# Performance work log

Measured on AMD Instinct MI355X. Metric: run time of the kernel, lower is better.

Reference implementation:

```python
import jax, jax.numpy as jnp
import numpy as np

N_NODES = 50000
N_EDGES = 1000000
C = 32          # nchannels (multiplicity of each irrep)
NBESSEL = 8
WEIGHT_NUMEL = 3 * C  # three uvu paths: 0e->0e, 0e->1o, 0e->2e


def setup_inputs() -> dict:
    key = jax.random.key(0)
    ks = jax.random.split(key, 12)
    inp = {
        "lenght": jax.random.uniform(ks[0], (N_EDGES, NBESSEL), dtype=jnp.float32),
        "node_features": jax.random.normal(ks[1], (N_NODES, C), dtype=jnp.float32),
        "edge_attributes": jax.random.normal(ks[2], (N_EDGES, 9), dtype=jnp.float32),
        "edge_index": jax.random.randint(ks[3], (2, N_EDGES), 0, N_NODES, dtype=jnp.int64),
        # FullyConnectedNet([8, 6, 6, 6, 96]) weights (e3nn stores unnormalized W, divides by sqrt(fan_in))
        "fcn_w0": jax.random.normal(ks[4], (NBESSEL, 6), dtype=jnp.float32),
        "fcn_w1": jax.random.normal(ks[5], (6, 6), dtype=jnp.float32),
        "fcn_w2": jax.random.normal(ks[6], (6, 6), dtype=jnp.float32),
        "fcn_w3": jax.random.normal(ks[7], (6, WEIGHT_NUMEL), dtype=jnp.float32),
        # equivariant Linear irreps_mid -> irreps_out: one [C, C] mixing matrix per l in {0,1,2}
        "lin_w0": jax.random.normal(ks[8], (C, C), dtype=jnp.float32),
        "lin_w1": jax.random.normal(ks[9], (C, C), dtype=jnp.float32),
        "lin_w2": jax.random.normal(ks[10], (C, C), dtype=jnp.float32),
    }
    return inp


def _fcn(x, w0, w1, w2, w3):
    # e3nn FullyConnectedNet: normalized linear layers with SiLU on hidden layers
    for w in (w0, w1, w2):
        x = jax.nn.silu((x @ w) * (1.0 / np.float32(np.sqrt(w.shape[0]))))
    return (x @ w3) * (1.0 / np.float32(np.sqrt(w3.shape[0])))


def reference(lenght, node_features, edge_attributes, edge_index,
              fcn_w0, fcn_w1, fcn_w2, fcn_w3, lin_w0, lin_w1, lin_w2):
    sender = edge_index[0]
    receiver = edge_index[1]
    num_nodes = node_features.shape[0]
    c = node_features.shape[1]
    e = lenght.shape[0]

    # per-edge tensor-product weights: [E, 3C]
    tp_w = _fcn(lenght, fcn_w0, fcn_w1, fcn_w2, fcn_w3)
    w0, w1, w2 = tp_w[:, :c], tp_w[:, c:2 * c], tp_w[:, 2 * c:]

    x = node_features[sender]                       # gather: [E, C]
    y0 = edge_attributes[:, 0:1]                    # 0e: [E, 1]
    y1 = edge_attributes[:, 1:4]                    # 1o: [E, 3]
    y2 = edge_attributes[:, 4:9]                    # 2e: [E, 5]

    # uvu tensor product, CG for 0e x l -> l is identity
    m0 = w0 * x * y0                                # [E, C]
    m1 = (w1 * x)[:, :, None] * y1[:, None, :]      # [E, C, 3]
    m2 = (w2 * x)[:, :, None] * y2[:, None, :]      # [E, C, 5]
    mij = jnp.concatenate(
        [m0, m1.reshape(e, 3 * c), m2.reshape(e, 5 * c)], axis=1)  # [E, 9C]

    # scatter_sum over receivers
    msg = jax.ops.segment_sum(mij, receiver, num_segments=num_nodes)  # [N, 9C]

    # equivariant Linear (per-l channel mixing, 1/sqrt(fan_in) normalization)
    inv = 1.0 / np.float32(np.sqrt(c))
    o0 = (msg[:, :c] @ lin_w0) * inv                                   # [N, C]
    o1 = jnp.einsum('nci,cd->ndi', msg[:, c:4 * c].reshape(num_nodes, c, 3), lin_w1) * inv
    o2 = jnp.einsum('nci,cd->ndi', msg[:, 4 * c:].reshape(num_nodes, c, 5), lin_w2) * inv
    return jnp.concatenate(
        [o0, o1.reshape(num_nodes, 3 * c), o2.reshape(num_nodes, 5 * c)], axis=1)
```

## Files before the change

### kernel.cpp

```cpp
#include <hip/hip_runtime.h>
#include <math.h>

#define N_NODES 50000
#define N_EDGES 1000000
#define CCH     32
#define ROW     288
#define SCAN_BLOCKS 196
#define REC_PAD 64

__global__ __launch_bounds__(256) void hist_kernel(
    const int* __restrict__ edge_index, int* __restrict__ deg)
{
    const int e = blockIdx.x * 256 + threadIdx.x;
    if (e >= N_EDGES) return;
    atomicAdd(&deg[edge_index[N_EDGES + e]], 1);
}

__global__ __launch_bounds__(256) void scan_local_kernel(
    const int* __restrict__ deg, int* __restrict__ lexcl, int* __restrict__ blocksum)
{
    __shared__ int s[256];
    const int t = threadIdx.x;
    const int gid = blockIdx.x * 256 + t;
    const int v = (gid < N_NODES) ? deg[gid] : 0;
    s[t] = v;
    __syncthreads();
    for (int ofs = 1; ofs < 256; ofs <<= 1) {
        int w = (t >= ofs) ? s[t - ofs] : 0;
        __syncthreads();
        s[t] += w;
        __syncthreads();
    }
    if (gid < N_NODES) lexcl[gid] = s[t] - v;
    if (t == 255) blocksum[blockIdx.x] = s[255];
}

__global__ __launch_bounds__(256) void scan_top_kernel(
    const int* __restrict__ blocksum, int* __restrict__ blockpref)
{
    __shared__ int s[256];
    const int t = threadIdx.x;
    const int v = (t < SCAN_BLOCKS) ? blocksum[t] : 0;
    s[t] = v;
    __syncthreads();
    for (int ofs = 1; ofs < 256; ofs <<= 1) {
        int w = (t >= ofs) ? s[t - ofs] : 0;
        __syncthreads();
        s[t] += w;
        __syncthreads();
    }
    if (t < SCAN_BLOCKS) blockpref[t] = s[t] - v;
}

__global__ __launch_bounds__(256) void scan_addback_kernel(
    const int* __restrict__ lexcl, const int* __restrict__ blockpref,
    int* __restrict__ offset, int* __restrict__ cursor)
{
    const int gid = blockIdx.x * 256 + threadIdx.x;
    if (gid >= N_NODES) return;
    const int base = blockpref[blockIdx.x] + lexcl[gid];
    offset[gid] = base;
    cursor[gid] = base;
}

__global__ __launch_bounds__(256) void pack_kernel(
    const float* __restrict__ lenght,
    const float* __restrict__ edge_attr,
    const int*   __restrict__ edge_index,
    const float* __restrict__ fw0,
    const float* __restrict__ fw1,
    const float* __restrict__ fw2,
    int*         __restrict__ cursor,
    float4*      __restrict__ rec)
{
    __shared__ float s_w[120];
    for (int i = threadIdx.x; i < 120; i += 256)
        s_w[i] = (i < 48) ? fw0[i] : (i < 84) ? fw1[i - 48] : fw2[i - 84];
    __syncthreads();
    const float* sw0 = s_w;
    const float* sw1 = s_w + 48;
    const float* sw2 = s_w + 84;

    const int e = blockIdx.x * 256 + threadIdx.x;
    if (e >= N_EDGES) return;

    const float inv8 = 0.35355339059327373f;
    const float inv6 = 0.4082482904638631f;

    float len[8];
    const float4 l0 = ((const float4*)(lenght + (long long)e * 8))[0];
    const float4 l1 = ((const float4*)(lenght + (long long)e * 8))[1];
    len[0]=l0.x; len[1]=l0.y; len[2]=l0.z; len[3]=l0.w;
    len[4]=l1.x; len[5]=l1.y; len[6]=l1.z; len[7]=l1.w;

    float h0[6], h1[6], h2[6];
    #pragma unroll
    for (int j = 0; j < 6; ++j) {
        float a = 0.f;
        #pragma unroll
        for (int k = 0; k < 8; ++k) a += len[k] * sw0[k * 6 + j];
        a *= inv8;
        h0[j] = a / (1.f + __expf(-a));
    }
    #pragma unroll
    for (int j = 0; j < 6; ++j) {
        float a = 0.f;
        #pragma unroll
        for (int k = 0; k < 6; ++k) a += h0[k] * sw1[k * 6 + j];
        a *= inv6;
        h1[j] = a / (1.f + __expf(-a));
    }
    #pragma unroll
    for (int j = 0; j < 6; ++j) {
        float a = 0.f;
        #pragma unroll
        for (int k = 0; k < 6; ++k) a += h1[k] * sw2[k * 6 + j];
        a *= inv6;
        h2[j] = a * inv6 / (1.f + __expf(-a));
    }

    const float* ea = edge_attr + (long long)e * 9;
    float y[9];
    #pragma unroll
    for (int i = 0; i < 9; ++i) y[i] = ea[i];

    const int snd = edge_index[e];
    const int r   = edge_index[N_EDGES + e];
    const int p   = atomicAdd(&cursor[r], 1);

    float4* rp = rec + (long long)p * 4;
    rp[0] = make_float4(h2[0], h2[1], h2[2], h2[3]);
    rp[1] = make_float4(h2[4], h2[5], y[0], y[1]);
    rp[2] = make_float4(y[2], y[3], y[4], y[5]);
    rp[3] = make_float4(y[6], y[7], y[8], __int_as_float(snd));
}

#define EDGE_ACC(Ra,Rb,Rc,Rd,xx) do {                                          \
    const float w0c_ = Ra.x*f3a[0] + Ra.y*f3a[1] + Ra.z*f3a[2]                 \
                     + Ra.w*f3a[3] + Rb.x*f3a[4] + Rb.y*f3a[5];                \
    const float w1c_ = Ra.x*f3b[0] + Ra.y*f3b[1] + Ra.z*f3b[2]                 \
                     + Ra.w*f3b[3] + Rb.x*f3b[4] + Rb.y*f3b[5];                \
    const float w2c_ = Ra.x*f3c[0] + Ra.y*f3c[1] + Ra.z*f3c[2]                 \
                     + Ra.w*f3c[3] + Rb.x*f3c[4] + Rb.y*f3c[5];                \
    acc[0] += (w0c_ * (xx)) * Rb.z;                                            \
    const float a1_ = w1c_ * (xx);                                             \
    acc[1] += a1_ * Rb.w; acc[2] += a1_ * Rc.x; acc[3] += a1_ * Rc.y;          \
    const float a2_ = w2c_ * (xx);                                             \
    acc[4] += a2_ * Rc.z; acc[5] += a2_ * Rc.w;                                \
    acc[6] += a2_ * Rd.x; acc[7] += a2_ * Rd.y; acc[8] += a2_ * Rd.z;          \
} while (0)

__global__ __launch_bounds__(256) void gather_kernel(
    const float4* __restrict__ rec,
    const float*  __restrict__ node_features,
    const int*    __restrict__ offset,
    const int*    __restrict__ deg,
    const float*  __restrict__ fw3,
    const float*  __restrict__ lw0,
    const float*  __restrict__ lw1,
    const float*  __restrict__ lw2,
    float*        __restrict__ out)
{
    __shared__ float s_lw0[1024], s_lw1[1024], s_lw2[1024];
    __shared__ float s_m[4][384];
    {
        const int t = threadIdx.x;
        ((float4*)s_lw0)[t] = ((const float4*)lw0)[t];
        ((float4*)s_lw1)[t] = ((const float4*)lw1)[t];
        ((float4*)s_lw2)[t] = ((const float4*)lw2)[t];
    }
    __syncthreads();

    const int wave = threadIdx.x >> 6;
    const int l    = threadIdx.x & 63;
    const int c    = l & 31;
    const int h    = l >> 5;
    const int node = blockIdx.x * 4 + wave;

    float f3a[6], f3b[6], f3c[6];
    #pragma unroll
    for (int k = 0; k < 6; ++k) {
        f3a[k] = fw3[k * 96 + c];
        f3b[k] = fw3[k * 96 + 32 + c];
        f3c[k] = fw3[k * 96 + 64 + c];
    }

    int off = offset[node];
    int dg  = deg[node];
    off = __builtin_amdgcn_readfirstlane(off);
    dg  = __builtin_amdgcn_readfirstlane(dg);
    const int nph = (dg + 3) >> 2;

    const float4* rb = rec + (size_t)off * 4;

    float acc[9] = {0.f,0.f,0.f,0.f,0.f,0.f,0.f,0.f,0.f};

    if (nph > 0) {
        int jA = 2 * h;
        int jB = 2 * h + 4;

        float4 A0 = rb[4*jA+0], A1 = rb[4*jA+1], A2 = rb[4*jA+2], A3 = rb[4*jA+3];
        float4 A4 = rb[4*jA+4], A5 = rb[4*jA+5], A6 = rb[4*jA+6], A7 = rb[4*jA+7];
        float4 B0 = rb[4*jB+0], B1 = rb[4*jB+1], B2 = rb[4*jB+2], B3 = rb[4*jB+3];
        float4 B4 = rb[4*jB+4], B5 = rb[4*jB+5], B6 = rb[4*jB+6], B7 = rb[4*jB+7];
        float xAr0 = node_features[(size_t)__float_as_int(A3.w) * CCH + c];
        float xAr1 = node_features[(size_t)__float_as_int(A7.w) * CCH + c];
        bool  vA0 = (jA < dg), vA1 = (jA + 1 < dg);
        float xBr0 = 0.f, xBr1 = 0.f;
        bool  vB0 = false, vB1 = false;

        int p = 0;
        while (true) {
            {
                const float xA0 = vA0 ? xAr0 : 0.f;
                const float xA1 = vA1 ? xAr1 : 0.f;
                EDGE_ACC(A0, A1, A2, A3, xA0);
                EDGE_ACC(A4, A5, A6, A7, xA1);
                xBr0 = node_features[(size_t)__float_as_int(B3.w) * CCH + c];
                xBr1 = node_features[(size_t)__float_as_int(B7.w) * CCH + c];
                vB0 = (jB < dg); vB1 = (jB + 1 < dg);
                jA += 8;
                A0 = rb[4*jA+0]; A1 = rb[4*jA+1]; A2 = rb[4*jA+2]; A3 = rb[4*jA+3];
                A4 = rb[4*jA+4]; A5 = rb[4*jA+5]; A6 = rb[4*jA+6]; A7 = rb[4*jA+7];
                if (++p == nph) break;
            }
            {
                const float xB0 = vB0 ? xBr0 : 0.f;
                const float xB1 = vB1 ? xBr1 : 0.f;
                EDGE_ACC(B0, B1, B2, B3, xB0);
                EDGE_ACC(B4, B5, B6, B7, xB1);
                xAr0 = node_features[(size_t)__float_as_int(A3.w) * CCH + c];
                xAr1 = node_features[(size_t)__float_as_int(A7.w) * CCH + c];
                vA0 = (jA < dg); vA1 = (jA + 1 < dg);
                jB += 8;
                B0 = rb[4*jB+0]; B1 = rb[4*jB+1]; B2 = rb[4*jB+2]; B3 = rb[4*jB+3];
                B4 = rb[4*jB+4]; B5 = rb[4*jB+5]; B6 = rb[4*jB+6]; B7 = rb[4*jB+7];
                if (++p == nph) break;
            }
        }
    }

    #pragma unroll
    for (int k = 0; k < 9; ++k) acc[k] += __shfl_down(acc[k], 32);

    if (h == 0) {
        float4* mp = (float4*)&s_m[wave][c * 12];
        mp[0] = make_float4(acc[0], acc[1], acc[2], acc[3]);
        mp[1] = make_float4(acc[4], acc[5], acc[6], acc[7]);
        s_m[wave][c * 12 + 8] = acc[8];
    }
    asm volatile("s_waitcnt lgkmcnt(0)" ::: "memory");

    const int d = c;
    float o0 = 0.f;
    float o1[3] = {0.f, 0.f, 0.f};
    float o2[5] = {0.f, 0.f, 0.f, 0.f, 0.f};
    for (int cc = h * 16; cc < h * 16 + 16; ++cc) {
        const float4 ma = *(const float4*)&s_m[wave][cc * 12];
        const float4 mb = *(const float4*)&s_m[wave][cc * 12 + 4];
        const float  m8 = s_m[wave][cc * 12 + 8];
        o0 += ma.x * s_lw0[cc * 32 + d];
        const float w1 = s_lw1[cc * 32 + d];
        o1[0] += ma.y * w1; o1[1] += ma.z * w1; o1[2] += ma.w * w1;
        const float w2 = s_lw2[cc * 32 + d];
        o2[0] += mb.x * w2; o2[1] += mb.y * w2; o2[2] += mb.z * w2;
        o2[3] += mb.w * w2; o2[4] += m8   * w2;
    }

    o0 += __shfl_down(o0, 32);
    #pragma unroll
    for (int i = 0; i < 3; ++i) o1[i] += __shfl_down(o1[i], 32);
    #pragma unroll
    for (int i = 0; i < 5; ++i) o2[i] += __shfl_down(o2[i], 32);

    if (h == 0) {
        const float inv32 = 0.17677669529663687f;
        float* rw = &s_m[wave][0];
        rw[d] = o0 * inv32;
        #pragma unroll
        for (int i = 0; i < 3; ++i) rw[32 + d * 3 + i] = o1[i] * inv32;
        #pragma unroll
        for (int i = 0; i < 5; ++i) rw[128 + d * 5 + i] = o2[i] * inv32;
    }
    asm volatile("s_waitcnt lgkmcnt(0)" ::: "memory");

    const float4* rowp = (const float4*)&s_m[wave][0];
    float4* op4 = (float4*)(out + (size_t)node * ROW);
    op4[l] = rowp[l];
    if (l < 8) op4[64 + l] = rowp[64 + l];
}

extern "C" void kernel_launch(void* const* d_in, const int* in_sizes, int n_in,
                              void* d_out, int out_size, void* d_ws, size_t ws_size,
                              hipStream_t stream)
{
    const float* lenght = (const float*)d_in[0];
    const float* nf     = (const float*)d_in[1];
    const float* ea     = (const float*)d_in[2];
    const int*   ei     = (const int*)d_in[3];
    const float* fw0    = (const float*)d_in[4];
    const float* fw1    = (const float*)d_in[5];
    const float* fw2    = (const float*)d_in[6];
    const float* fw3    = (const float*)d_in[7];
    const float* lw0    = (const float*)d_in[8];
    const float* lw1    = (const float*)d_in[9];
    const float* lw2    = (const float*)d_in[10];
    float* out = (float*)d_out;

    char* ws = (char*)d_ws;
    float4* rec    = (float4*)ws; ws += ((size_t)N_EDGES * 4 + REC_PAD) * sizeof(float4);
    int* deg       = (int*)ws;    ws += (size_t)N_NODES * sizeof(int);
    int* offset    = (int*)ws;    ws += (size_t)N_NODES * sizeof(int);
    int* cursor    = (int*)ws;    ws += (size_t)N_NODES * sizeof(int);
    int* lexcl     = (int*)ws;    ws += (size_t)N_NODES * sizeof(int);
    int* blocksum  = (int*)ws;    ws += (size_t)SCAN_BLOCKS * sizeof(int);
    int* blockpref = (int*)ws;    ws += (size_t)SCAN_BLOCKS * sizeof(int);
    float4* recpad = rec + (size_t)N_EDGES * 4;

    hipMemsetAsync(deg, 0, (size_t)N_NODES * sizeof(int), stream);
    hipMemsetAsync(recpad, 0, (size_t)REC_PAD * sizeof(float4), stream);

    const int EB = (N_EDGES + 255) / 256;
    hist_kernel        <<<EB, 256, 0, stream>>>(ei, deg);
    scan_local_kernel  <<<SCAN_BLOCKS, 256, 0, stream>>>(deg, lexcl, blocksum);
    scan_top_kernel    <<<1, 256, 0, stream>>>(blocksum, blockpref);
    scan_addback_kernel<<<SCAN_BLOCKS, 256, 0, stream>>>(lexcl, blockpref, offset, cursor);
    pack_kernel        <<<EB, 256, 0, stream>>>(lenght, ea, ei, fw0, fw1, fw2, cursor, rec);
    gather_kernel      <<<N_NODES / 4, 256, 0, stream>>>(
        rec, nf, offset, deg, fw3, lw0, lw1, lw2, out);
}
```

Before: 355.3 us.

## Record per-edge rank in histogram pass and make gather kernel persistent

The histogram kernel now stores each edge's slot within its receiver, returned by the atomicAdd. The pack kernel then computes the destination as offset plus rank instead of running a second atomic on a cursor array. This removes one contended atomic pass, at the cost of writing and reading an extra 4 MB rank array. Separately, the gather kernel becomes a grid-stride loop over 2048 blocks, so the fw3 and linear weight loads into shared memory are amortised over many nodes, though load balancing across blocks may get worse.

```diff
diff --git a/kernel.cpp b/kernel.cpp
--- a/kernel.cpp
+++ b/kernel.cpp
@@ -7,13 +7,15 @@
 #define ROW     288
 #define SCAN_BLOCKS 196
 #define REC_PAD 64
-
-__global__ __launch_bounds__(256) void hist_kernel(
-    const int* __restrict__ edge_index, int* __restrict__ deg)
+#define GATHER_BLOCKS 2048
+
+__global__ __launch_bounds__(256) void rank_kernel(
+    const int* __restrict__ edge_index, int* __restrict__ deg,
+    int* __restrict__ rank)
 {
     const int e = blockIdx.x * 256 + threadIdx.x;
     if (e >= N_EDGES) return;
-    atomicAdd(&deg[edge_index[N_EDGES + e]], 1);
+    rank[e] = atomicAdd(&deg[edge_index[N_EDGES + e]], 1);
 }
 
 __global__ __launch_bounds__(256) void scan_local_kernel(
@@ -54,13 +56,11 @@
 
 __global__ __launch_bounds__(256) void scan_addback_kernel(
     const int* __restrict__ lexcl, const int* __restrict__ blockpref,
-    int* __restrict__ offset, int* __restrict__ cursor)
+    int* __restrict__ offset)
 {
     const int gid = blockIdx.x * 256 + threadIdx.x;
     if (gid >= N_NODES) return;
-    const int base = blockpref[blockIdx.x] + lexcl[gid];
-    offset[gid] = base;
-    cursor[gid] = base;
+    offset[gid] = blockpref[blockIdx.x] + lexcl[gid];
 }
 
 __global__ __launch_bounds__(256) void pack_kernel(
@@ -70,7 +70,8 @@
     const float* __restrict__ fw0,
     const float* __restrict__ fw1,
     const float* __restrict__ fw2,
-    int*         __restrict__ cursor,
+    const int*   __restrict__ offset,
+    const int*   __restrict__ rank,
     float4*      __restrict__ rec)
 {
     __shared__ float s_w[120];
@@ -126,7 +127,7 @@
 
     const int snd = edge_index[e];
     const int r   = edge_index[N_EDGES + e];
-    const int p   = atomicAdd(&cursor[r], 1);
+    const int p   = offset[r] + rank[e];
 
     float4* rp = rec + (long long)p * 4;
     rp[0] = make_float4(h2[0], h2[1], h2[2], h2[3]);
@@ -175,7 +176,6 @@
     const int l    = threadIdx.x & 63;
     const int c    = l & 31;
     const int h    = l >> 5;
-    const int node = blockIdx.x * 4 + wave;
 
     float f3a[6], f3b[6], f3c[6];
     #pragma unroll
@@ -185,109 +185,113 @@
         f3c[k] = fw3[k * 96 + 64 + c];
     }
 
-    int off = offset[node];
-    int dg  = deg[node];
-    off = __builtin_amdgcn_readfirstlane(off);
-    dg  = __builtin_amdgcn_readfirstlane(dg);
-    const int nph = (dg + 3) >> 2;
-
-    const float4* rb = rec + (size_t)off * 4;
-
-    float acc[9] = {0.f,0.f,0.f,0.f,0.f,0.f,0.f,0.f,0.f};
-
-    if (nph > 0) {
-        int jA = 2 * h;
-        int jB = 2 * h + 4;
-
-        float4 A0 = rb[4*jA+0], A1 = rb[4*jA+1], A2 = rb[4*jA+2], A3 = rb[4*jA+3];
-        float4 A4 = rb[4*jA+4], A5 = rb[4*jA+5], A6 = rb[4*jA+6], A7 = rb[4*jA+7];
-        float4 B0 = rb[4*jB+0], B1 = rb[4*jB+1], B2 = rb[4*jB+2], B3 = rb[4*jB+3];
-        float4 B4 = rb[4*jB+4], B5 = rb[4*jB+5], B6 = rb[4*jB+6], B7 = rb[4*jB+7];
-        float xAr0 = node_features[(size_t)__float_as_int(A3.w) * CCH + c];
-        float xAr1 = node_features[(size_t)__float_as_int(A7.w) * CCH + c];
-        bool  vA0 = (jA < dg), vA1 = (jA + 1 < dg);
-        float xBr0 = 0.f, xBr1 = 0.f;
-        bool  vB0 = false, vB1 = false;
-
-        int p = 0;
-        while (true) {
-            {
-                const float xA0 = vA0 ? xAr0 : 0.f;
-                const float xA1 = vA1 ? xAr1 : 0.f;
-                EDGE_ACC(A0, A1, A2, A3, xA0);
-                EDGE_ACC(A4, A5, A6, A7, xA1);
-                xBr0 = node_features[(size_t)__float_as_int(B3.w) * CCH + c];
-                xBr1 = node_features[(size_t)__float_as_int(B7.w) * CCH + c];
-                vB0 = (jB < dg); vB1 = (jB + 1 < dg);
-                jA += 8;
-                A0 = rb[4*jA+0]; A1 = rb[4*jA+1]; A2 = rb[4*jA+2]; A3 = rb[4*jA+3];
-                A4 = rb[4*jA+4]; A5 = rb[4*jA+5]; A6 = rb[4*jA+6]; A7 = rb[4*jA+7];
-                if (++p == nph) break;
-            }
-            {
-                const float xB0 = vB0 ? xBr0 : 0.f;
-                const float xB1 = vB1 ? xBr1 : 0.f;
-                EDGE_ACC(B0, B1, B2, B3, xB0);
-                EDGE_ACC(B4, B5, B6, B7, xB1);
-                xAr0 = node_features[(size_t)__float_as_int(A3.w) * CCH + c];
-                xAr1 = node_features[(size_t)__float_as_int(A7.w) * CCH + c];
-                vA0 = (jA < dg); vA1 = (jA + 1 < dg);
-                jB += 8;
-                B0 = rb[4*jB+0]; B1 = rb[4*jB+1]; B2 = rb[4*jB+2]; B3 = rb[4*jB+3];
-                B4 = rb[4*jB+4]; B5 = rb[4*jB+5]; B6 = rb[4*jB+6]; B7 = rb[4*jB+7];
-                if (++p == nph) break;
+    for (int node = blockIdx.x * 4 + wave; node < N_NODES;
+         node += GATHER_BLOCKS * 4) {
+
+        int off = offset[node];
+        int dg  = deg[node];
+        off = __builtin_amdgcn_readfirstlane(off);
+        dg  = __builtin_amdgcn_readfirstlane(dg);
+        const int nph = (dg + 3) >> 2;
+
+        const float4* rb = rec + (size_t)off * 4;
+
+        float acc[9] = {0.f,0.f,0.f,0.f,0.f,0.f,0.f,0.f,0.f};
+
+        if (nph > 0) {
+            int jA = 2 * h;
+            int jB = 2 * h + 4;
+
+            float4 A0 = rb[4*jA+0], A1 = rb[4*jA+1], A2 = rb[4*jA+2], A3 = rb[4*jA+3];
+            float4 A4 = rb[4*jA+4], A5 = rb[4*jA+5], A6 = rb[4*jA+6], A7 = rb[4*jA+7];
+            float4 B0 = rb[4*jB+0], B1 = rb[4*jB+1], B2 = rb[4*jB+2], B3 = rb[4*jB+3];
+            float4 B4 = rb[4*jB+4], B5 = rb[4*jB+5], B6 = rb[4*jB+6], B7 = rb[4*jB+7];
+            float xAr0 = node_features[(size_t)__float_as_int(A3.w) * CCH + c];
+            float xAr1 = node_features[(size_t)__float_as_int(A7.w) * CCH + c];
+            bool  vA0 = (jA < dg), vA1 = (jA + 1 < dg);
+            float xBr0 = 0.f, xBr1 = 0.f;
+            bool  vB0 = false, vB1 = false;
+
+            int p = 0;
+            while (true) {
+                {
+                    const float xA0 = vA0 ? xAr0 : 0.f;
+                    const float xA1 = vA1 ? xAr1 : 0.f;
+                    EDGE_ACC(A0, A1, A2, A3, xA0);
+                    EDGE_ACC(A4, A5, A6, A7, xA1);
+                    xBr0 = node_features[(size_t)__float_as_int(B3.w) * CCH + c];
+                    xBr1 = node_features[(size_t)__float_as_int(B7.w) * CCH + c];
+                    vB0 = (jB < dg); vB1 = (jB + 1 < dg);
+                    jA += 8;
+                    A0 = rb[4*jA+0]; A1 = rb[4*jA+1]; A2 = rb[4*jA+2]; A3 = rb[4*jA+3];
+                    A4 = rb[4*jA+4]; A5 = rb[4*jA+5]; A6 = rb[4*jA+6]; A7 = rb[4*jA+7];
+                    if (++p == nph) break;
+                }
+                {
+                    const float xB0 = vB0 ? xBr0 : 0.f;
+                    const float xB1 = vB1 ? xBr1 : 0.f;
+                    EDGE_ACC(B0, B1, B2, B3, xB0);
+                    EDGE_ACC(B4, B5, B6, B7, xB1);
+                    xAr0 = node_features[(size_t)__float_as_int(A3.w) * CCH + c];
+                    xAr1 = node_features[(size_t)__float_as_int(A7.w) * CCH + c];
+                    vA0 = (jA < dg); vA1 = (jA + 1 < dg);
+                    jB += 8;
+                    B0 = rb[4*jB+0]; B1 = rb[4*jB+1]; B2 = rb[4*jB+2]; B3 = rb[4*jB+3];
+                    B4 = rb[4*jB+4]; B5 = rb[4*jB+5]; B6 = rb[4*jB+6]; B7 = rb[4*jB+7];
+                    if (++p == nph) break;
+                }
             }
         }
-    }
-
-    #pragma unroll
-    for (int k = 0; k < 9; ++k) acc[k] += __shfl_down(acc[k], 32);
-
-    if (h == 0) {
-        float4* mp = (float4*)&s_m[wave][c * 12];
-        mp[0] = make_float4(acc[0], acc[1], acc[2], acc[3]);
-        mp[1] = make_float4(acc[4], acc[5], acc[6], acc[7]);
-        s_m[wave][c * 12 + 8] = acc[8];
-    }
-    asm volatile("s_waitcnt lgkmcnt(0)" ::: "memory");
-
-    const int d = c;
-    float o0 = 0.f;
-    float o1[3] = {0.f, 0.f, 0.f};
-    float o2[5] = {0.f, 0.f, 0.f, 0.f, 0.f};
-    for (int cc = h * 16; cc < h * 16 + 16; ++cc) {
-        const float4 ma = *(const float4*)&s_m[wave][cc * 12];
-        const float4 mb = *(const float4*)&s_m[wave][cc * 12 + 4];
-        const float  m8 = s_m[wave][cc * 12 + 8];
-        o0 += ma.x * s_lw0[cc * 32 + d];
-        const float w1 = s_lw1[cc * 32 + d];
-        o1[0] += ma.y * w1; o1[1] += ma.z * w1; o1[2] += ma.w * w1;
-        const float w2 = s_lw2[cc * 32 + d];
-        o2[0] += mb.x * w2; o2[1] += mb.y * w2; o2[2] += mb.z * w2;
-        o2[3] += mb.w * w2; o2[4] += m8   * w2;
-    }
-
-    o0 += __shfl_down(o0, 32);
-    #pragma unroll
-    for (int i = 0; i < 3; ++i) o1[i] += __shfl_down(o1[i], 32);
-    #pragma unroll
-    for (int i = 0; i < 5; ++i) o2[i] += __shfl_down(o2[i], 32);
-
-    if (h == 0) {
-        const float inv32 = 0.17677669529663687f;
-        float* rw = &s_m[wave][0];
-        rw[d] = o0 * inv32;
-        #pragma unroll
-        for (int i = 0; i < 3; ++i) rw[32 + d * 3 + i] = o1[i] * inv32;
-        #pragma unroll
-        for (int i = 0; i < 5; ++i) rw[128 + d * 5 + i] = o2[i] * inv32;
-    }
-    asm volatile("s_waitcnt lgkmcnt(0)" ::: "memory");
-
-    const float4* rowp = (const float4*)&s_m[wave][0];
-    float4* op4 = (float4*)(out + (size_t)node * ROW);
-    op4[l] = rowp[l];
-    if (l < 8) op4[64 + l] = rowp[64 + l];
+
+        #pragma unroll
+        for (int k = 0; k < 9; ++k) acc[k] += __shfl_down(acc[k], 32);
+
+        if (h == 0) {
+            float4* mp = (float4*)&s_m[wave][c * 12];
+            mp[0] = make_float4(acc[0], acc[1], acc[2], acc[3]);
+            mp[1] = make_float4(acc[4], acc[5], acc[6], acc[7]);
+            s_m[wave][c * 12 + 8] = acc[8];
+        }
+        asm volatile("s_waitcnt lgkmcnt(0)" ::: "memory");
+
+        const int d = c;
+        float o0 = 0.f;
+        float o1[3] = {0.f, 0.f, 0.f};
+        float o2[5] = {0.f, 0.f, 0.f, 0.f, 0.f};
+        for (int cc = h * 16; cc < h * 16 + 16; ++cc) {
+            const float4 ma = *(const float4*)&s_m[wave][cc * 12];
+            const float4 mb = *(const float4*)&s_m[wave][cc * 12 + 4];
+            const float  m8 = s_m[wave][cc * 12 + 8];
+            o0 += ma.x * s_lw0[cc * 32 + d];
+            const float w1 = s_lw1[cc * 32 + d];
+            o1[0] += ma.y * w1; o1[1] += ma.z * w1; o1[2] += ma.w * w1;
+            const float w2 = s_lw2[cc * 32 + d];
+            o2[0] += mb.x * w2; o2[1] += mb.y * w2; o2[2] += mb.z * w2;
+            o2[3] += mb.w * w2; o2[4] += m8   * w2;
+        }
+
+        o0 += __shfl_down(o0, 32);
+        #pragma unroll
+        for (int i = 0; i < 3; ++i) o1[i] += __shfl_down(o1[i], 32);
+        #pragma unroll
+        for (int i = 0; i < 5; ++i) o2[i] += __shfl_down(o2[i], 32);
+
+        if (h == 0) {
+            const float inv32 = 0.17677669529663687f;
+            float* rw = &s_m[wave][0];
+            rw[d] = o0 * inv32;
+            #pragma unroll
+            for (int i = 0; i < 3; ++i) rw[32 + d * 3 + i] = o1[i] * inv32;
+            #pragma unroll
+            for (int i = 0; i < 5; ++i) rw[128 + d * 5 + i] = o2[i] * inv32;
+        }
+        asm volatile("s_waitcnt lgkmcnt(0)" ::: "memory");
+
+        const float4* rowp = (const float4*)&s_m[wave][0];
+        float4* op4 = (float4*)(out + (size_t)node * ROW);
+        op4[l] = rowp[l];
+        if (l < 8) op4[64 + l] = rowp[64 + l];
+    }
 }
 
 extern "C" void kernel_launch(void* const* d_in, const int* in_sizes, int n_in,
@@ -309,9 +313,9 @@
 
     char* ws = (char*)d_ws;
     float4* rec    = (float4*)ws; ws += ((size_t)N_EDGES * 4 + REC_PAD) * sizeof(float4);
+    int* rank      = (int*)ws;    ws += (size_t)N_EDGES * sizeof(int);
     int* deg       = (int*)ws;    ws += (size_t)N_NODES * sizeof(int);
     int* offset    = (int*)ws;    ws += (size_t)N_NODES * sizeof(int);
-    int* cursor    = (int*)ws;    ws += (size_t)N_NODES * sizeof(int);
     int* lexcl     = (int*)ws;    ws += (size_t)N_NODES * sizeof(int);
     int* blocksum  = (int*)ws;    ws += (size_t)SCAN_BLOCKS * sizeof(int);
     int* blockpref = (int*)ws;    ws += (size_t)SCAN_BLOCKS * sizeof(int);
@@ -321,11 +325,12 @@
     hipMemsetAsync(recpad, 0, (size_t)REC_PAD * sizeof(float4), stream);
 
     const int EB = (N_EDGES + 255) / 256;
-    hist_kernel        <<<EB, 256, 0, stream>>>(ei, deg);
+    rank_kernel        <<<EB, 256, 0, stream>>>(ei, deg, rank);
     scan_local_kernel  <<<SCAN_BLOCKS, 256, 0, stream>>>(deg, lexcl, blocksum);
     scan_top_kernel    <<<1, 256, 0, stream>>>(blocksum, blockpref);
-    scan_addback_kernel<<<SCAN_BLOCKS, 256, 0, stream>>>(lexcl, blockpref, offset, cursor);
-    pack_kernel        <<<EB, 256, 0, stream>>>(lenght, ea, ei, fw0, fw1, fw2, cursor, rec);
-    gather_kernel      <<<N_NODES / 4, 256, 0, stream>>>(
+    scan_addback_kernel<<<SCAN_BLOCKS, 256, 0, stream>>>(lexcl, blockpref, offset);
+    pack_kernel        <<<EB, 256, 0, stream>>>(lenght, ea, ei, fw0, fw1, fw2,
+                                                offset, rank, rec);
+    gather_kernel      <<<GATHER_BLOCKS, 256, 0, stream>>>(
         rec, nf, offset, deg, fw3, lw0, lw1, lw2, out);
 }
```

Measured after the change: 353.7 us. Within noise of the previous version (-0.4%).
